# Optimization experiments

Hardware: AMD Instinct MI355X
Metric: run time of the kernel (lower is better)

The kernel has to match this reference:

```python
import jax, jax.numpy as jnp
import numpy as np

B, T, F, U, P = 64, 4096, 128, 128, 16  # batch, timesteps, filters, units, skip


def setup_inputs() -> dict:
    key = jax.random.key(0)
    k1, k2, k3, k4 = jax.random.split(key, 4)
    inputs = jax.random.normal(k1, (B, T, F), dtype=jnp.float32)
    # Keras GRUCell params (reset_after=True, default): kernel [F,3U],
    # recurrent_kernel [U,3U], bias [2,3U] (input bias + recurrent bias).
    kernel = jax.random.normal(k2, (F, 3 * U), dtype=jnp.float32) * (1.0 / np.sqrt(F))
    recurrent_kernel = jax.random.normal(k3, (U, 3 * U), dtype=jnp.float32) * (1.0 / np.sqrt(U))
    bias = jax.random.normal(k4, (2, 3 * U), dtype=jnp.float32) * 0.01
    return {"inputs": inputs, "kernel": kernel,
            "recurrent_kernel": recurrent_kernel, "bias": bias}


def reference(inputs, kernel, recurrent_kernel, bias):
    # SkipGRU: h[t] = GRUCell(x[t], h[t-P]) with h[t]=GRUCell(x[t], 0) for t<P.
    # This factorizes into P independent GRU chains of length T//P, which we
    # fold into the batch axis and run with one lax.scan.
    Bs, Ts, Fs = inputs.shape
    Us = recurrent_kernel.shape[0]
    Ls = Ts // P  # chain length
    # [B,T,F] -> [B,L,P,F] -> [B,P,L,F] -> [B*P,L,F]; chain j holds steps t=l*P+j
    x = inputs.reshape(Bs, Ls, P, Fs).transpose(0, 2, 1, 3).reshape(Bs * P, Ls, Fs)
    b_in, b_rec = bias[0], bias[1]
    # Precompute input projections for all steps: [B*P, L, 3U]
    xm = jnp.einsum('blf,fu->blu', x, kernel) + b_in

    def step(h, xt):
        hm = h @ recurrent_kernel + b_rec              # [B*P, 3U]
        z = jax.nn.sigmoid(xt[:, :Us] + hm[:, :Us])
        r = jax.nn.sigmoid(xt[:, Us:2 * Us] + hm[:, Us:2 * Us])
        hh = jax.nn.relu(xt[:, 2 * Us:] + r * hm[:, 2 * Us:])  # activation='relu'
        h_new = z * h + (1.0 - z) * hh
        return h_new, h_new

    h0 = jnp.zeros((Bs * P, Us), dtype=inputs.dtype)
    _, outs = jax.lax.scan(step, h0, xm.transpose(1, 0, 2))  # outs: [L, B*P, U]
    # [L,B*P,U] -> [B,P,L,U] -> [B,L,P,U] -> [B,T,U] (return_sequences=True)
    outs = outs.transpose(1, 0, 2).reshape(Bs, P, Ls, Us)
    outs = outs.transpose(0, 2, 1, 3).reshape(Bs, Ts, Us)
    return outs
```

## Files before the change

### kernel.cpp

```cpp
#include <hip/hip_runtime.h>
#include <hip/hip_bf16.h>


#define B_N 64
#define T_N 4096
#define F_N 128
#define U_N 128
#define P_N 16
#define L_N 256
#define NW 8
#define NT (NW * 64)

typedef _Float16 f16x8 __attribute__((ext_vector_type(8)));
typedef _Float16 f16x4 __attribute__((ext_vector_type(4)));
typedef float f32x4 __attribute__((ext_vector_type(4)));

__device__ __forceinline__ float sigmoidf_(float x) {
    return __builtin_amdgcn_rcpf(1.0f + __expf(-x));
}

#define BAR() do { \
    asm volatile("s_waitcnt lgkmcnt(0)" ::: "memory"); \
    __builtin_amdgcn_s_barrier(); \
    __builtin_amdgcn_sched_barrier(0); \
} while (0)

__global__ __launch_bounds__(NT, 2) void skipgru_kernel(
    const float* __restrict__ xg, const float* __restrict__ Wk,
    const float* __restrict__ Wr, const float* __restrict__ bias,
    float* __restrict__ out)
{
    __shared__ __align__(16) _Float16 A_x[2][16][132];
    __shared__ __align__(16) _Float16 A_h[2][16][132];

    const int tid  = threadIdx.x;
    const int lane = tid & 63;
    const int wave = tid >> 6;
    const int ln   = lane & 15;
    const int lg   = lane >> 4;
    const int u    = wave * 16 + ln;
    const int m0   = lg * 4;
    const int b    = blockIdx.x;

    const float bz  = bias[u]       + bias[384 + u];
    const float br  = bias[128 + u] + bias[384 + 128 + u];
    const float bxh = bias[256 + u];
    const float brh = bias[384 + 256 + u];

    f16x8 wzk[4], wzr[4], wrk[4], wrr[4], whk[4], whr[4];
    #pragma unroll
    for (int kt = 0; kt < 4; ++kt) {
        #pragma unroll
        for (int e = 0; e < 8; ++e) {
            int k = kt * 32 + ((e >> 2) << 4) + (lg << 2) + (e & 3);
            const float* wkp = Wk + (size_t)k * 384;
            const float* wrp = Wr + (size_t)k * 384;
            wzk[kt][e] = (_Float16)wkp[u];
            wzr[kt][e] = (_Float16)wrp[u];
            wrk[kt][e] = (_Float16)wkp[128 + u];
            wrr[kt][e] = (_Float16)wrp[128 + u];
            whk[kt][e] = (_Float16)wkp[256 + u];
            whr[kt][e] = (_Float16)wrp[256 + u];
        }
    }

    for (int q = tid; q < 16 * 132; q += NT) ((_Float16*)A_h[0])[q] = (_Float16)0;

    const int sm = tid & 15, sc = (tid >> 4) << 2;
    const float* xb = xg + (size_t)b * T_N * F_N;
    {
        float4 x0 = *(const float4*)(xb + (size_t)sm * F_N + sc);
        f16x4 v = {(_Float16)x0.x, (_Float16)x0.y, (_Float16)x0.z, (_Float16)x0.w};
        *(f16x4*)&A_x[0][sm][sc] = v;
    }
    float4 xsB = *(const float4*)(xb + (size_t)(P_N + sm) * F_N + sc);
    float4 xsA = *(const float4*)(xb + (size_t)(2 * P_N + sm) * F_N + sc);

    f32x4 hreg = {0.f, 0.f, 0.f, 0.f};
    __syncthreads();

    auto step = [&](int l, float4& xs) {
        const int cur = l & 1, nxt = (l + 1) & 1;
        f16x8 axf[4], ahf[4];
        #pragma unroll
        for (int kt = 0; kt < 4; ++kt) {
            f16x4 lo = *(const f16x4*)&A_x[cur][ln][kt * 32 + 4 * lg];
            f16x4 hi = *(const f16x4*)&A_x[cur][ln][kt * 32 + 4 * lg + 16];
            axf[kt] = __builtin_shufflevector(lo, hi, 0, 1, 2, 3, 4, 5, 6, 7);
            f16x4 lo2 = *(const f16x4*)&A_h[cur][ln][kt * 32 + 4 * lg];
            f16x4 hi2 = *(const f16x4*)&A_h[cur][ln][kt * 32 + 4 * lg + 16];
            ahf[kt] = __builtin_shufflevector(lo2, hi2, 0, 1, 2, 3, 4, 5, 6, 7);
        }
        f32x4 azx = {bz, bz, bz, bz}, azh = {0.f, 0.f, 0.f, 0.f};
        f32x4 arx = {br, br, br, br}, arh = {0.f, 0.f, 0.f, 0.f};
        f32x4 axh = {bxh, bxh, bxh, bxh}, ahh = {brh, brh, brh, brh};
        #pragma unroll
        for (int kt = 0; kt < 4; ++kt) {
            azx = __builtin_amdgcn_mfma_f32_16x16x32_f16(axf[kt], wzk[kt], azx, 0, 0, 0);
            arx = __builtin_amdgcn_mfma_f32_16x16x32_f16(axf[kt], wrk[kt], arx, 0, 0, 0);
            axh = __builtin_amdgcn_mfma_f32_16x16x32_f16(axf[kt], whk[kt], axh, 0, 0, 0);
            azh = __builtin_amdgcn_mfma_f32_16x16x32_f16(ahf[kt], wzr[kt], azh, 0, 0, 0);
            arh = __builtin_amdgcn_mfma_f32_16x16x32_f16(ahf[kt], wrr[kt], arh, 0, 0, 0);
            ahh = __builtin_amdgcn_mfma_f32_16x16x32_f16(ahf[kt], whr[kt], ahh, 0, 0, 0);
        }
        float* op = out + ((size_t)b * T_N + (size_t)l * P_N + m0) * U_N + u;
        #pragma unroll
        for (int e = 0; e < 4; ++e) {
            float z = sigmoidf_(azx[e] + azh[e]);
            float r = sigmoidf_(arx[e] + arh[e]);
            float c = fmaxf(0.f, axh[e] + r * ahh[e]);
            float hn = z * hreg[e] + (1.f - z) * c;
            hreg[e] = hn;
            A_h[nxt][m0 + e][u] = (_Float16)hn;
            op[(size_t)e * U_N] = hn;
        }
        if (l + 1 < L_N) {
            f16x4 v = {(_Float16)xs.x, (_Float16)xs.y, (_Float16)xs.z, (_Float16)xs.w};
            *(f16x4*)&A_x[nxt][sm][sc] = v;
            int t = l + 3;
            if (t < L_N)
                xs = *(const float4*)(xb + (size_t)(t * P_N + sm) * F_N + sc);
        }
        BAR();
    };

    for (int l = 0; l < L_N; l += 2) {
        step(l, xsB);
        step(l + 1, xsA);
    }
}

extern "C" void kernel_launch(void* const* d_in, const int* in_sizes, int n_in,
                              void* d_out, int out_size, void* d_ws, size_t ws_size,
                              hipStream_t stream) {
    const float* inputs = (const float*)d_in[0];
    const float* kernel = (const float*)d_in[1];
    const float* rker   = (const float*)d_in[2];
    const float* bias   = (const float*)d_in[3];
    float* o = (float*)d_out;
    hipLaunchKernelGGL(skipgru_kernel, dim3(B_N), dim3(NT), 0, stream,
                       inputs, kernel, rker, bias, o);
}
```

Before: 204.3 us.

## Pipeline input projection one step ahead and permute LDS layout for vector loads

The input-projection MFMAs for step l+1 are computed during step l, after the recurrent MFMAs, and folded into the accumulators that the recurrent MFMAs then add to. This takes the x-projection off the serial h-dependence chain and leaves only the recurrent matmul in it. The LDS columns are permuted so each lane's 8 fp16 operands are contiguous, replacing two 4-wide reads plus a shuffle with a single 8-wide read. The gate math is also folded into fmas, and the x prefetch distance grows by one step, which raises register pressure.

```diff
diff --git a/kernel.cpp b/kernel.cpp
--- a/kernel.cpp
+++ b/kernel.cpp
@@ -19,11 +19,17 @@
     return __builtin_amdgcn_rcpf(1.0f + __expf(-x));
 }
 
+__device__ __forceinline__ int fpos(int k) {
+    return ((k >> 5) << 5) + (((k >> 2) & 3) << 3) + (((k >> 4) & 1) << 2) + (k & 3);
+}
+
 #define BAR() do { \
     asm volatile("s_waitcnt lgkmcnt(0)" ::: "memory"); \
     __builtin_amdgcn_s_barrier(); \
     __builtin_amdgcn_sched_barrier(0); \
 } while (0)
+
+struct Acc { f32x4 z, r, xh, hh; };
 
 __global__ __launch_bounds__(NT, 2) void skipgru_kernel(
     const float* __restrict__ xg, const float* __restrict__ Wk,
@@ -41,6 +47,7 @@
     const int u    = wave * 16 + ln;
     const int m0   = lg * 4;
     const int b    = blockIdx.x;
+    const int hcol = fpos(u);
 
     const float bz  = bias[u]       + bias[384 + u];
     const float br  = bias[128 + u] + bias[384 + 128 + u];
@@ -67,66 +74,92 @@
     for (int q = tid; q < 16 * 132; q += NT) ((_Float16*)A_h[0])[q] = (_Float16)0;
 
     const int sm = tid & 15, sc = (tid >> 4) << 2;
+    const int scp = fpos(sc);
     const float* xb = xg + (size_t)b * T_N * F_N;
     {
         float4 x0 = *(const float4*)(xb + (size_t)sm * F_N + sc);
-        f16x4 v = {(_Float16)x0.x, (_Float16)x0.y, (_Float16)x0.z, (_Float16)x0.w};
-        *(f16x4*)&A_x[0][sm][sc] = v;
+        float4 x1 = *(const float4*)(xb + (size_t)(P_N + sm) * F_N + sc);
+        f16x4 v0 = {(_Float16)x0.x, (_Float16)x0.y, (_Float16)x0.z, (_Float16)x0.w};
+        f16x4 v1 = {(_Float16)x1.x, (_Float16)x1.y, (_Float16)x1.z, (_Float16)x1.w};
+        *(f16x4*)&A_x[0][sm][scp] = v0;
+        *(f16x4*)&A_x[1][sm][scp] = v1;
     }
-    float4 xsB = *(const float4*)(xb + (size_t)(P_N + sm) * F_N + sc);
-    float4 xsA = *(const float4*)(xb + (size_t)(2 * P_N + sm) * F_N + sc);
+    float4 xsB = *(const float4*)(xb + (size_t)(2 * P_N + sm) * F_N + sc);
+    float4 xsA = *(const float4*)(xb + (size_t)(3 * P_N + sm) * F_N + sc);
 
     f32x4 hreg = {0.f, 0.f, 0.f, 0.f};
+    float* op = out + ((size_t)b * T_N + m0) * U_N + u;
     __syncthreads();
 
-    auto step = [&](int l, float4& xs) {
-        const int cur = l & 1, nxt = (l + 1) & 1;
-        f16x8 axf[4], ahf[4];
+    Acc P, Q;
+    {
+        f16x8 axf[4];
+        #pragma unroll
+        for (int kt = 0; kt < 4; ++kt)
+            axf[kt] = *(const f16x8*)&A_x[0][ln][kt * 32 + lg * 8];
+        P.z  = {bz, bz, bz, bz};
+        P.r  = {br, br, br, br};
+        P.xh = {bxh, bxh, bxh, bxh};
+        P.hh = {brh, brh, brh, brh};
         #pragma unroll
         for (int kt = 0; kt < 4; ++kt) {
-            f16x4 lo = *(const f16x4*)&A_x[cur][ln][kt * 32 + 4 * lg];
-            f16x4 hi = *(const f16x4*)&A_x[cur][ln][kt * 32 + 4 * lg + 16];
-            axf[kt] = __builtin_shufflevector(lo, hi, 0, 1, 2, 3, 4, 5, 6, 7);
-            f16x4 lo2 = *(const f16x4*)&A_h[cur][ln][kt * 32 + 4 * lg];
-            f16x4 hi2 = *(const f16x4*)&A_h[cur][ln][kt * 32 + 4 * lg + 16];
-            ahf[kt] = __builtin_shufflevector(lo2, hi2, 0, 1, 2, 3, 4, 5, 6, 7);
+            P.z  = __builtin_amdgcn_mfma_f32_16x16x32_f16(axf[kt], wzk[kt], P.z, 0, 0, 0);
+            P.r  = __builtin_amdgcn_mfma_f32_16x16x32_f16(axf[kt], wrk[kt], P.r, 0, 0, 0);
+            P.xh = __builtin_amdgcn_mfma_f32_16x16x32_f16(axf[kt], whk[kt], P.xh, 0, 0, 0);
         }
-        f32x4 azx = {bz, bz, bz, bz}, azh = {0.f, 0.f, 0.f, 0.f};
-        f32x4 arx = {br, br, br, br}, arh = {0.f, 0.f, 0.f, 0.f};
-        f32x4 axh = {bxh, bxh, bxh, bxh}, ahh = {brh, brh, brh, brh};
+    }
+
+    auto step = [&](int l, float4& xs, Acc& cur, Acc& nxt) {
+        const int rbuf = l & 1, wbuf = (l + 1) & 1;
+        f16x8 ahf[4];
+        #pragma unroll
+        for (int kt = 0; kt < 4; ++kt)
+            ahf[kt] = *(const f16x8*)&A_h[rbuf][ln][kt * 32 + lg * 8];
         #pragma unroll
         for (int kt = 0; kt < 4; ++kt) {
-            azx = __builtin_amdgcn_mfma_f32_16x16x32_f16(axf[kt], wzk[kt], azx, 0, 0, 0);
-            arx = __builtin_amdgcn_mfma_f32_16x16x32_f16(axf[kt], wrk[kt], arx, 0, 0, 0);
-            axh = __builtin_amdgcn_mfma_f32_16x16x32_f16(axf[kt], whk[kt], axh, 0, 0, 0);
-            azh = __builtin_amdgcn_mfma_f32_16x16x32_f16(ahf[kt], wzr[kt], azh, 0, 0, 0);
-            arh = __builtin_amdgcn_mfma_f32_16x16x32_f16(ahf[kt], wrr[kt], arh, 0, 0, 0);
-            ahh = __builtin_amdgcn_mfma_f32_16x16x32_f16(ahf[kt], whr[kt], ahh, 0, 0, 0);
+            cur.z  = __builtin_amdgcn_mfma_f32_16x16x32_f16(ahf[kt], wzr[kt], cur.z, 0, 0, 0);
+            cur.r  = __builtin_amdgcn_mfma_f32_16x16x32_f16(ahf[kt], wrr[kt], cur.r, 0, 0, 0);
+            cur.hh = __builtin_amdgcn_mfma_f32_16x16x32_f16(ahf[kt], whr[kt], cur.hh, 0, 0, 0);
         }
-        float* op = out + ((size_t)b * T_N + (size_t)l * P_N + m0) * U_N + u;
+        if (l + 1 < L_N) {
+            f16x8 axf[4];
+            #pragma unroll
+            for (int kt = 0; kt < 4; ++kt)
+                axf[kt] = *(const f16x8*)&A_x[wbuf][ln][kt * 32 + lg * 8];
+            nxt.z  = {bz, bz, bz, bz};
+            nxt.r  = {br, br, br, br};
+            nxt.xh = {bxh, bxh, bxh, bxh};
+            nxt.hh = {brh, brh, brh, brh};
+            #pragma unroll
+            for (int kt = 0; kt < 4; ++kt) {
+                nxt.z  = __builtin_amdgcn_mfma_f32_16x16x32_f16(axf[kt], wzk[kt], nxt.z, 0, 0, 0);
+                nxt.r  = __builtin_amdgcn_mfma_f32_16x16x32_f16(axf[kt], wrk[kt], nxt.r, 0, 0, 0);
+                nxt.xh = __builtin_amdgcn_mfma_f32_16x16x32_f16(axf[kt], whk[kt], nxt.xh, 0, 0, 0);
+            }
+        }
         #pragma unroll
         for (int e = 0; e < 4; ++e) {
-            float z = sigmoidf_(azx[e] + azh[e]);
-            float r = sigmoidf_(arx[e] + arh[e]);
-            float c = fmaxf(0.f, axh[e] + r * ahh[e]);
-            float hn = z * hreg[e] + (1.f - z) * c;
+            float z = sigmoidf_(cur.z[e]);
+            float r = sigmoidf_(cur.r[e]);
+            float c = fmaxf(0.f, fmaf(r, cur.hh[e], cur.xh[e]));
+            float hn = fmaf(z, hreg[e] - c, c);
             hreg[e] = hn;
-            A_h[nxt][m0 + e][u] = (_Float16)hn;
+            A_h[wbuf][m0 + e][hcol] = (_Float16)hn;
             op[(size_t)e * U_N] = hn;
         }
-        if (l + 1 < L_N) {
+        op += P_N * U_N;
+        if (l + 2 < L_N) {
             f16x4 v = {(_Float16)xs.x, (_Float16)xs.y, (_Float16)xs.z, (_Float16)xs.w};
-            *(f16x4*)&A_x[nxt][sm][sc] = v;
-            int t = l + 3;
-            if (t < L_N)
-                xs = *(const float4*)(xb + (size_t)(t * P_N + sm) * F_N + sc);
+            *(f16x4*)&A_x[rbuf][sm][scp] = v;
+            if (l + 4 < L_N)
+                xs = *(const float4*)(xb + (size_t)((l + 4) * P_N + sm) * F_N + sc);
         }
         BAR();
     };
 
     for (int l = 0; l < L_N; l += 2) {
-        step(l, xsB);
-        step(l + 1, xsA);
+        step(l, xsB, P, Q);
+        step(l + 1, xsA, Q, P);
     }
 }
 
```

Result: faster. 186.5 us (-8.7%).
